# Kernel optimization log

Measured on AMD Instinct MI355X. Metric: run time of the kernel, lower is better.

The kernel has to match this reference:

```python
import jax, jax.numpy as jnp
import numpy as np

N_DRUG = 50000
N_PROT = 50000
N_EDGE = 800000
D_IN = 256
D_HID = 256
D_OUT = 128


def setup_inputs() -> dict:
    key = jax.random.key(0)
    ks = jax.random.split(key, 20)
    s_in = 1.0 / np.sqrt(D_IN)
    inp = {
        'x_drug': jax.random.normal(ks[0], (N_DRUG, D_IN), jnp.float32),
        'x_protein': jax.random.normal(ks[1], (N_PROT, D_IN), jnp.float32),
        'edge_dp': jnp.stack([
            jax.random.randint(ks[2], (N_EDGE,), 0, N_DRUG, jnp.int32),
            jax.random.randint(ks[3], (N_EDGE,), 0, N_PROT, jnp.int32)]),
        'edge_pd': jnp.stack([
            jax.random.randint(ks[4], (N_EDGE,), 0, N_PROT, jnp.int32),
            jax.random.randint(ks[5], (N_EDGE,), 0, N_DRUG, jnp.int32)]),
        'W1l_dp': jax.random.normal(ks[6], (D_IN, D_HID), jnp.float32) * s_in,
        'W1r_dp': jax.random.normal(ks[7], (D_IN, D_HID), jnp.float32) * s_in,
        'b1_dp': jnp.zeros((D_HID,), jnp.float32),
        'W1l_pd': jax.random.normal(ks[8], (D_IN, D_HID), jnp.float32) * s_in,
        'W1r_pd': jax.random.normal(ks[9], (D_IN, D_HID), jnp.float32) * s_in,
        'b1_pd': jnp.zeros((D_HID,), jnp.float32),
        'W2l_dp': jax.random.normal(ks[10], (D_HID, D_OUT), jnp.float32) / np.sqrt(D_HID),
        'W2r_dp': jax.random.normal(ks[11], (D_HID, D_OUT), jnp.float32) / np.sqrt(D_HID),
        'b2_dp': jnp.zeros((D_OUT,), jnp.float32),
        'W2l_pd': jax.random.normal(ks[12], (D_HID, D_OUT), jnp.float32) / np.sqrt(D_HID),
        'W2r_pd': jax.random.normal(ks[13], (D_HID, D_OUT), jnp.float32) / np.sqrt(D_HID),
        'b2_pd': jnp.zeros((D_OUT,), jnp.float32),
    }
    return inp


def _sage(x_src, x_dst, edge, Wl, Wr, b):
    """PyG SAGEConv (mean aggr): lin_l(mean_neighbors) + lin_r(x_dst) + bias."""
    src, dst = edge[0], edge[1]
    n_dst = x_dst.shape[0]
    msg = x_src[src]                                        # [E, d] gather
    s = jax.ops.segment_sum(msg, dst, num_segments=n_dst)   # [n_dst, d]
    cnt = jax.ops.segment_sum(jnp.ones((edge.shape[1],), x_src.dtype), dst,
                              num_segments=n_dst)
    mean = s / jnp.maximum(cnt, 1.0)[:, None]
    return mean @ Wl + x_dst @ Wr + b


def _l2norm(x, eps=1e-12):
    n = jnp.sqrt(jnp.sum(x * x, axis=-1, keepdims=True))
    return x / jnp.maximum(n, eps)


def reference(x_drug, x_protein, edge_dp, edge_pd,
              W1l_dp, W1r_dp, b1_dp, W1l_pd, W1r_pd, b1_pd,
              W2l_dp, W2r_dp, b2_dp, W2l_pd, W2r_pd, b2_pd):
    # Layer 1 (HeteroConv, aggr='sum'; each node type has one incoming edge type)
    h_prot = _sage(x_drug, x_protein, edge_dp, W1l_dp, W1r_dp, b1_dp)
    h_drug = _sage(x_protein, x_drug, edge_pd, W1l_pd, W1r_pd, b1_pd)
    h_prot = jax.nn.relu(h_prot)  # dropout is identity in eval mode
    h_drug = jax.nn.relu(h_drug)
    # Layer 2 (output layer) + L2 normalize
    z_prot = _sage(h_drug, h_prot, edge_dp, W2l_dp, W2r_dp, b2_dp)
    z_drug = _sage(h_prot, h_drug, edge_pd, W2l_pd, W2r_pd, b2_pd)
    return _l2norm(z_drug), _l2norm(z_prot)
```

## Files before the change

### kernel.cpp

```cpp
#include <hip/hip_runtime.h>

typedef unsigned short u16;
typedef unsigned int u32;
typedef __attribute__((ext_vector_type(8))) short short8;
typedef __attribute__((ext_vector_type(4))) float f32x4;

#define NDIM 256
#define KCAT 512
#define EB 8192
#define NBK_MAX 256

__device__ __forceinline__ float bf2f(u16 u) {
  union { u32 i; float f; } v; v.i = ((u32)u) << 16; return v.f;
}
__device__ __forceinline__ u16 f2bf(float f) {
  union { float f; u32 i; } v; v.f = f;
  u32 u = v.i;
  u32 r = (u + 0x7fffu + ((u >> 16) & 1u)) >> 16;
  return (u16)r;
}

__global__ void cvt_f32_bf16_2(const float* __restrict__ a, int n4a,
                               const float* __restrict__ b, int n4b,
                               u16* __restrict__ oa, u16* __restrict__ ob) {
  int i = blockIdx.x * blockDim.x + threadIdx.x;
  const float* in; u16* out; int j;
  if (i < n4a) { in = a; out = oa; j = i; }
  else { j = i - n4a; if (j >= n4b) return; in = b; out = ob; }
  const float4 v = reinterpret_cast<const float4*>(in)[j];
  u32 lo = (u32)f2bf(v.x) | ((u32)f2bf(v.y) << 16);
  u32 hi = (u32)f2bf(v.z) | ((u32)f2bf(v.w) << 16);
  reinterpret_cast<uint2*>(out)[j] = make_uint2(lo, hi);
}

__global__ void prep_wcat(const float* __restrict__ Wl0, const float* __restrict__ Wr0,
                          u16* __restrict__ WT0,
                          const float* __restrict__ Wl1, const float* __restrict__ Wr1,
                          u16* __restrict__ WT1) {
  int idx = blockIdx.x * blockDim.x + threadIdx.x;
  if (idx >= 256 * KCAT) return;
  const float* Wl = blockIdx.y ? Wl1 : Wl0;
  const float* Wr = blockIdx.y ? Wr1 : Wr0;
  u16* WT = blockIdx.y ? WT1 : WT0;
  int n = idx >> 9, k = idx & 511;
  float v = (k < 256) ? Wl[k * 256 + n] : Wr[(k - 256) * 256 + n];
  WT[idx] = f2bf(v);
}

__global__ void prep_wcat2(const float* __restrict__ Wl0, const float* __restrict__ Wr0,
                           u16* __restrict__ WT0,
                           const float* __restrict__ Wl1, const float* __restrict__ Wr1,
                           u16* __restrict__ WT1) {
  int idx = blockIdx.x * blockDim.x + threadIdx.x;
  if (idx >= 256 * 256) return;
  const float* Wl = blockIdx.y ? Wl1 : Wl0;
  const float* Wr = blockIdx.y ? Wr1 : Wr0;
  u16* WT = blockIdx.y ? WT1 : WT0;
  int n = idx >> 8, k = idx & 255;
  float v = (n < 128) ? Wl[k * 128 + n] : Wr[k * 128 + (n - 128)];
  WT[idx] = f2bf(v);
}

__global__ void prep_fbias(const float* __restrict__ bd, const float* __restrict__ bp,
                           float* __restrict__ fd, float* __restrict__ fp) {
  int n = threadIdx.x;
  fd[n] = (n < 128) ? 0.f : bd[n - 128];
  fp[n] = (n < 128) ? 0.f : bp[n - 128];
}

#define SCAN_CHUNK 2048

__global__ void scan_p1(const int* __restrict__ c0, int n0,
                        const int* __restrict__ c1, int n1,
                        int* __restrict__ bsums) {
  const int sel = blockIdx.y;
  const int* c = sel ? c1 : c0;
  const int n = sel ? n1 : n0;
  const int base = blockIdx.x * SCAN_CHUNK;
  const int tid = threadIdx.x, lane = tid & 63, w = tid >> 6;
  int s = 0;
  const int i0 = base + tid * 8;
#pragma unroll
  for (int j = 0; j < 8; ++j) {
    int i = i0 + j;
    s += (i < n) ? c[i] : 0;
  }
#pragma unroll
  for (int d = 1; d < 64; d <<= 1) s += __shfl_xor(s, d, 64);
  __shared__ int wsum[4];
  if (lane == 0) wsum[w] = s;
  __syncthreads();
  if (tid == 0) bsums[sel * 64 + blockIdx.x] = wsum[0] + wsum[1] + wsum[2] + wsum[3];
}

__global__ void scan_p2(int* __restrict__ bsums, int nb) {
  const int sel = blockIdx.x;
  const int lane = threadIdx.x;
  int v = (lane < nb) ? bsums[sel * 64 + lane] : 0;
#pragma unroll
  for (int d = 1; d < 64; d <<= 1) {
    int t = __shfl_up(v, d, 64);
    if (lane >= d) v += t;
  }
  int ex = __shfl_up(v, 1, 64);
  if (lane == 0) ex = 0;
  if (lane < nb) bsums[sel * 64 + lane] = ex;
}

__global__ void scan_p3(const int* __restrict__ c0, int n0, int* __restrict__ off0,
                        const int* __restrict__ c1, int n1, int* __restrict__ off1,
                        const int* __restrict__ bsums) {
  const int sel = blockIdx.y;
  const int* c = sel ? c1 : c0;
  int* off = sel ? off1 : off0;
  const int n = sel ? n1 : n0;
  const int base = blockIdx.x * SCAN_CHUNK;
  const int tid = threadIdx.x, lane = tid & 63, w = tid >> 6;
  int v[8];
  int s = 0;
  const int i0 = base + tid * 8;
#pragma unroll
  for (int j = 0; j < 8; ++j) {
    int i = i0 + j;
    v[j] = (i < n) ? c[i] : 0;
    s += v[j];
  }
  int inc = s;
#pragma unroll
  for (int d = 1; d < 64; d <<= 1) {
    int t = __shfl_up(inc, d, 64);
    if (lane >= d) inc += t;
  }
  __shared__ int wsum[4];
  if (lane == 63) wsum[w] = inc;
  __syncthreads();
  int wbase = 0;
  for (int q = 0; q < w; ++q) wbase += wsum[q];
  int run = (inc - s) + wbase + bsums[sel * 64 + blockIdx.x];
#pragma unroll
  for (int j = 0; j < 8; ++j) {
    int i = i0 + j;
    run += v[j];
    if (i < n) off[i + 1] = run;
  }
  if (blockIdx.x == 0 && tid == 0) off[0] = 0;
}

__global__ void hist_pass(const int* __restrict__ d0, const int* __restrict__ d1, int E,
                          int nblk, int nbuckets, int* __restrict__ h0, int* __restrict__ h1) {
  const int sel = blockIdx.y;
  const int* dst = sel ? d1 : d0;
  int* hist = sel ? h1 : h0;
  const int blk = blockIdx.x;
  __shared__ int h[NBK_MAX];
  for (int b = threadIdx.x; b < nbuckets; b += 256) h[b] = 0;
  __syncthreads();
  const int e0 = blk * EB;
  const int e1 = (e0 + EB < E) ? (e0 + EB) : E;
  for (int i = e0 + threadIdx.x; i < e1; i += 256) atomicAdd(&h[dst[i] >> 8], 1);
  __syncthreads();
  for (int b = threadIdx.x; b < nbuckets; b += 256) hist[b * nblk + blk] = h[b];
}

__global__ void part_pass(const int* __restrict__ s0, const int* __restrict__ d0, u32* __restrict__ t0,
                          const int* __restrict__ s1, const int* __restrict__ d1, u32* __restrict__ t1,
                          const int* __restrict__ ho0, const int* __restrict__ ho1,
                          int E, int nblk, int nbuckets) {
  const int sel = blockIdx.y;
  const int* src = sel ? s1 : s0;
  const int* dst = sel ? d1 : d0;
  const int* hoff = sel ? ho1 : ho0;
  u32* tmp = sel ? t1 : t0;
  const int blk = blockIdx.x;
  __shared__ int cur[NBK_MAX];
  for (int b = threadIdx.x; b < nbuckets; b += 256) cur[b] = hoff[b * nblk + blk];
  __syncthreads();
  const int e0 = blk * EB;
  const int e1 = (e0 + EB < E) ? (e0 + EB) : E;
  for (int i = e0 + threadIdx.x; i < e1; i += 256) {
    const int d = dst[i];
    const int p = atomicAdd(&cur[d >> 8], 1);
    tmp[p] = ((u32)(d & 255) << 16) | (u32)src[i];
  }
}

__global__ void bucket_fill(const u32* __restrict__ t0, const int* __restrict__ ho0,
                            int n0, int* __restrict__ off0, int* __restrict__ l0,
                            const u32* __restrict__ t1, const int* __restrict__ ho1,
                            int n1, int* __restrict__ off1, int* __restrict__ l1,
                            int E, int nblk, int nbuckets) {
  const int sel = blockIdx.y;
  const u32* tmp = sel ? t1 : t0;
  const int* hoff = sel ? ho1 : ho0;
  const int n = sel ? n1 : n0;
  int* off = sel ? off1 : off0;
  int* lst = sel ? l1 : l0;
  const int b = blockIdx.x;
  const int node0 = b << 8;
  if (node0 >= n) return;
  const int nodes = (n - node0 < 256) ? (n - node0) : 256;
  const int base = hoff[b * nblk];
  const int bend = hoff[(b + 1) * nblk];
  const int t = threadIdx.x, lane = t & 63, w = t >> 6;
  __shared__ int cnt[256];
  __shared__ int wsum[4];
  cnt[t] = 0;
  __syncthreads();
  for (int i = base + t; i < bend; i += 256) atomicAdd(&cnt[tmp[i] >> 16], 1);
  __syncthreads();
  const int v = cnt[t];
  int inc = v;
#pragma unroll
  for (int d = 1; d < 64; d <<= 1) {
    int x = __shfl_up(inc, d, 64);
    if (lane >= d) inc += x;
  }
  if (lane == 63) wsum[w] = inc;
  __syncthreads();
  int wb = 0;
  for (int q = 0; q < w; ++q) wb += wsum[q];
  const int excl = base + (inc - v) + wb;
  __syncthreads();
  cnt[t] = excl;
  if (t < nodes) off[node0 + t] = excl;
  if (node0 + nodes == n && t == 0) off[n] = E;
  __syncthreads();
  for (int i = base + t; i < bend; i += 256) {
    const u32 pk = tmp[i];
    const int p = atomicAdd(&cnt[pk >> 16], 1);
    lst[p] = (int)(pk & 0xffffu);
  }
}

__global__ void seg_mean(const u16* __restrict__ f0, const int* __restrict__ o0,
                         const int* __restrict__ l0, u16* __restrict__ out0, int n0,
                         const u16* __restrict__ f1, const int* __restrict__ o1,
                         const int* __restrict__ l1, u16* __restrict__ out1, int n1) {
  const int sel = blockIdx.y;
  const u16* feat = sel ? f1 : f0;
  const int* off = sel ? o1 : o0;
  const int* lst = sel ? l1 : l0;
  u16* out = sel ? out1 : out0;
  const int ndst = sel ? n1 : n0;
  const int wid = threadIdx.x >> 6, lane = threadIdx.x & 63;
  const int node = blockIdx.x * 4 + wid;
  if (node >= ndst) return;
  const int s = off[node], e = off[node + 1];
  const int half = lane >> 5, hl = lane & 31;
  float a[8];
#pragma unroll
  for (int j = 0; j < 8; ++j) a[j] = 0.f;
  int i = s;
  for (; i + 8 <= e; i += 8) {
    const int q0 = lst[i + half], q1 = lst[i + 2 + half];
    const int q2 = lst[i + 4 + half], q3 = lst[i + 6 + half];
    const uint4 v0 = *reinterpret_cast<const uint4*>(feat + (size_t)q0 * NDIM + hl * 8);
    const uint4 v1 = *reinterpret_cast<const uint4*>(feat + (size_t)q1 * NDIM + hl * 8);
    const uint4 v2 = *reinterpret_cast<const uint4*>(feat + (size_t)q2 * NDIM + hl * 8);
    const uint4 v3 = *reinterpret_cast<const uint4*>(feat + (size_t)q3 * NDIM + hl * 8);
    const u32 w0[4] = {v0.x, v0.y, v0.z, v0.w};
    const u32 w1[4] = {v1.x, v1.y, v1.z, v1.w};
    const u32 w2[4] = {v2.x, v2.y, v2.z, v2.w};
    const u32 w3[4] = {v3.x, v3.y, v3.z, v3.w};
#pragma unroll
    for (int q = 0; q < 4; ++q) {
      a[2 * q] += bf2f((u16)(w0[q] & 0xffffu)) + bf2f((u16)(w1[q] & 0xffffu)) +
                  bf2f((u16)(w2[q] & 0xffffu)) + bf2f((u16)(w3[q] & 0xffffu));
      a[2 * q + 1] += bf2f((u16)(w0[q] >> 16)) + bf2f((u16)(w1[q] >> 16)) +
                      bf2f((u16)(w2[q] >> 16)) + bf2f((u16)(w3[q] >> 16));
    }
  }
  for (; i < e; i += 2) {
    if (i + half < e) {
      const int q = lst[i + half];
      const uint4 v = *reinterpret_cast<const uint4*>(feat + (size_t)q * NDIM + hl * 8);
      const u32 w[4] = {v.x, v.y, v.z, v.w};
#pragma unroll
      for (int t = 0; t < 4; ++t) {
        a[2 * t] += bf2f((u16)(w[t] & 0xffffu));
        a[2 * t + 1] += bf2f((u16)(w[t] >> 16));
      }
    }
  }
#pragma unroll
  for (int j = 0; j < 8; ++j) a[j] += __shfl_xor(a[j], 32, 64);
  if (half == 0) {
    const float inv = (e > s) ? 1.f / (float)(e - s) : 0.f;
    uint4 o;
    o.x = (u32)f2bf(a[0] * inv) | ((u32)f2bf(a[1] * inv) << 16);
    o.y = (u32)f2bf(a[2] * inv) | ((u32)f2bf(a[3] * inv) << 16);
    o.z = (u32)f2bf(a[4] * inv) | ((u32)f2bf(a[5] * inv) << 16);
    o.w = (u32)f2bf(a[6] * inv) | ((u32)f2bf(a[7] * inv) << 16);
    *reinterpret_cast<uint4*>(out + (size_t)node * NDIM + hl * 8) = o;
  }
}

__global__ void seg_out(const u16* __restrict__ ym0, const u16* __restrict__ ys0,
                        const int* __restrict__ o0, const int* __restrict__ l0,
                        float* __restrict__ z0, int n0,
                        const u16* __restrict__ ym1, const u16* __restrict__ ys1,
                        const int* __restrict__ o1, const int* __restrict__ l1,
                        float* __restrict__ z1, int n1) {
  const int sel = blockIdx.y;
  const u16* ymsg = sel ? ym1 : ym0;
  const u16* yself = sel ? ys1 : ys0;
  const int* off = sel ? o1 : o0;
  const int* lst = sel ? l1 : l0;
  float* zout = sel ? z1 : z0;
  const int ndst = sel ? n1 : n0;
  const int wid = threadIdx.x >> 6, lane = threadIdx.x & 63;
  const int node = blockIdx.x * 4 + wid;
  if (node >= ndst) return;
  const int s = off[node], e = off[node + 1];
  const int q = lane >> 4, ql = lane & 15;
  float a[8];
#pragma unroll
  for (int j = 0; j < 8; ++j) a[j] = 0.f;
  int i = s;
  for (; i + 8 <= e; i += 8) {
    const int r0 = lst[i + q], r1 = lst[i + 4 + q];
    const uint4 v0 = *reinterpret_cast<const uint4*>(ymsg + (size_t)r0 * 128 + ql * 8);
    const uint4 v1 = *reinterpret_cast<const uint4*>(ymsg + (size_t)r1 * 128 + ql * 8);
    const u32 w0[4] = {v0.x, v0.y, v0.z, v0.w};
    const u32 w1[4] = {v1.x, v1.y, v1.z, v1.w};
#pragma unroll
    for (int c = 0; c < 4; ++c) {
      a[2 * c] += bf2f((u16)(w0[c] & 0xffffu)) + bf2f((u16)(w1[c] & 0xffffu));
      a[2 * c + 1] += bf2f((u16)(w0[c] >> 16)) + bf2f((u16)(w1[c] >> 16));
    }
  }
  for (; i + 4 <= e; i += 4) {
    const int r = lst[i + q];
    const uint4 v = *reinterpret_cast<const uint4*>(ymsg + (size_t)r * 128 + ql * 8);
    const u32 w[4] = {v.x, v.y, v.z, v.w};
#pragma unroll
    for (int c = 0; c < 4; ++c) {
      a[2 * c] += bf2f((u16)(w[c] & 0xffffu));
      a[2 * c + 1] += bf2f((u16)(w[c] >> 16));
    }
  }
  if (i + q < e) {
    const int r = lst[i + q];
    const uint4 v = *reinterpret_cast<const uint4*>(ymsg + (size_t)r * 128 + ql * 8);
    const u32 w[4] = {v.x, v.y, v.z, v.w};
#pragma unroll
    for (int c = 0; c < 4; ++c) {
      a[2 * c] += bf2f((u16)(w[c] & 0xffffu));
      a[2 * c + 1] += bf2f((u16)(w[c] >> 16));
    }
  }
#pragma unroll
  for (int j = 0; j < 8; ++j) {
    a[j] += __shfl_xor(a[j], 16, 64);
    a[j] += __shfl_xor(a[j], 32, 64);
  }
  const float inv = (e > s) ? 1.f / (float)(e - s) : 0.f;
  const uint4 r = *reinterpret_cast<const uint4*>(yself + (size_t)node * 128 + ql * 8);
  const u32 rw[4] = {r.x, r.y, r.z, r.w};
  float z[8];
  float ss = 0.f;
#pragma unroll
  for (int c = 0; c < 4; ++c) {
    z[2 * c] = a[2 * c] * inv + bf2f((u16)(rw[c] & 0xffffu));
    z[2 * c + 1] = a[2 * c + 1] * inv + bf2f((u16)(rw[c] >> 16));
    ss += z[2 * c] * z[2 * c] + z[2 * c + 1] * z[2 * c + 1];
  }
#pragma unroll
  for (int d = 1; d < 16; d <<= 1) ss += __shfl_xor(ss, d, 64);
  const float sc = 1.f / fmaxf(sqrtf(ss), 1e-12f);
  if (q == 0) {
    float4 o0v, o1v;
    o0v.x = z[0] * sc; o0v.y = z[1] * sc; o0v.z = z[2] * sc; o0v.w = z[3] * sc;
    o1v.x = z[4] * sc; o1v.y = z[5] * sc; o1v.z = z[6] * sc; o1v.w = z[7] * sc;
    float* zp = zout + (size_t)node * 128 + ql * 8;
    *reinterpret_cast<float4*>(zp) = o0v;
    *reinterpret_cast<float4*>(zp + 4) = o1v;
  }
}

template <bool RELU, bool CAT, int KT, bool SPLIT>
__global__ __launch_bounds__(256) void gemm2(
    const u16* __restrict__ Am0, const u16* __restrict__ Ax0,
    const u16* __restrict__ WT0, const float* __restrict__ bias0,
    u16* __restrict__ out0, u16* __restrict__ outs0, int M0,
    const u16* __restrict__ Am1, const u16* __restrict__ Ax1,
    const u16* __restrict__ WT1, const float* __restrict__ bias1,
    u16* __restrict__ out1, u16* __restrict__ outs1, int M1,
    int gx, int ldb, int ldo) {
  const int raw = blockIdx.x;
  const int xcd = raw & 7, seq = raw >> 3;
  const int ny = seq & 1;
  const int mt = (seq >> 1) * 8 + xcd;
  if (mt >= gx) return;
  const int sel = blockIdx.z;
  const u16* Am = sel ? Am1 : Am0;
  const u16* Ax = sel ? Ax1 : Ax0;
  const u16* WT = sel ? WT1 : WT0;
  const float* bias = sel ? bias1 : bias0;
  u16* out = sel ? out1 : out0;
  u16* outs = sel ? outs1 : outs0;
  const int M = sel ? M1 : M0;
  const int gm0 = mt * 128;
  if (gm0 >= M) return;
  const int n0 = ny * 128;

  __shared__ u16 As[8192];
  __shared__ u16 Bs[8192];
  const int tid = threadIdx.x;
  const int wid = tid >> 6, lane = tid & 63;
  const int wr = wid >> 1, wc = wid & 1;

  f32x4 acc[4][4];
  const f32x4 zz = {0.f, 0.f, 0.f, 0.f};
#pragma unroll
  for (int i = 0; i < 4; ++i)
#pragma unroll
    for (int j = 0; j < 4; ++j) acc[i][j] = zz;

  for (int kt = 0; kt < KT; ++kt) {
    const u16* Asrc = CAT ? ((kt < KT / 2) ? Am : Ax) : Am;
    const int koff = CAT ? ((kt & (KT / 2 - 1)) * 64) : kt * 64;
#pragma unroll
    for (int t = 0; t < 4; ++t) {
      const int f = wid * 256 + t * 64 + lane;
      const int row = f >> 3;
      const int ch = (f & 7) ^ (row & 7);
      int grow = gm0 + row; grow = (grow < M) ? grow : (M - 1);
      const u16* g = Asrc + (size_t)grow * NDIM + koff + ch * 8;
      u16* l = &As[(size_t)f * 8];
      __builtin_amdgcn_global_load_lds((const __attribute__((address_space(1))) void*)g,
                                       (__attribute__((address_space(3))) void*)l, 16, 0, 0);
    }
#pragma unroll
    for (int t = 0; t < 4; ++t) {
      const int f = wid * 256 + t * 64 + lane;
      const int n = f >> 3;
      const int ch = (f & 7) ^ (n & 7);
      const u16* g = WT + (size_t)(n0 + n) * ldb + kt * 64 + ch * 8;
      u16* l = &Bs[(size_t)f * 8];
      __builtin_amdgcn_global_load_lds((const __attribute__((address_space(1))) void*)g,
                                       (__attribute__((address_space(3))) void*)l, 16, 0, 0);
    }
    __syncthreads();
#pragma unroll
    for (int ks = 0; ks < 2; ++ks) {
      const int kc = ks * 4 + (lane >> 4);
      short8 a[4], b[4];
#pragma unroll
      for (int mtt = 0; mtt < 4; ++mtt) {
        const int R = wr * 64 + mtt * 16 + (lane & 15);
        a[mtt] = *reinterpret_cast<const short8*>(&As[(size_t)R * 64 + (kc ^ (R & 7)) * 8]);
      }
#pragma unroll
      for (int nt = 0; nt < 4; ++nt) {
        const int N = wc * 64 + nt * 16 + (lane & 15);
        b[nt] = *reinterpret_cast<const short8*>(&Bs[(size_t)N * 64 + (kc ^ (N & 7)) * 8]);
      }
#pragma unroll
      for (int mtt = 0; mtt < 4; ++mtt)
#pragma unroll
        for (int nt = 0; nt < 4; ++nt)
          acc[mtt][nt] = __builtin_amdgcn_mfma_f32_16x16x32_bf16(a[mtt], b[nt], acc[mtt][nt], 0, 0, 0);
    }
    __syncthreads();
  }

  const int rw = gm0 + wr * 64;
#pragma unroll
  for (int mtt = 0; mtt < 4; ++mtt) {
#pragma unroll
    for (int j = 0; j < 4; ++j) {
      int row = rw + mtt * 16 + ((lane >> 4) << 2) + j;
      if (row >= M) continue;
#pragma unroll
      for (int nt = 0; nt < 4; ++nt) {
        int col = n0 + wc * 64 + nt * 16 + (lane & 15);
        float v = acc[mtt][nt][j] + bias[col];
        if (RELU) v = fmaxf(v, 0.f);
        if constexpr (SPLIT) {
          if (col < 128) out[(size_t)row * 128 + col] = f2bf(v);
          else outs[(size_t)row * 128 + col - 128] = f2bf(v);
        } else {
          out[(size_t)row * ldo + col] = f2bf(v);
        }
      }
    }
  }
}

extern "C" void kernel_launch(void* const* d_in, const int* in_sizes, int n_in,
                              void* d_out, int out_size, void* d_ws, size_t ws_size,
                              hipStream_t stream) {
  const float* x_drug = (const float*)d_in[0];
  const float* x_prot = (const float*)d_in[1];
  const int* e_dp = (const int*)d_in[2];
  const int* e_pd = (const int*)d_in[3];
  const float* W1l_dp = (const float*)d_in[4];
  const float* W1r_dp = (const float*)d_in[5];
  const float* b1_dp = (const float*)d_in[6];
  const float* W1l_pd = (const float*)d_in[7];
  const float* W1r_pd = (const float*)d_in[8];
  const float* b1_pd = (const float*)d_in[9];
  const float* W2l_dp = (const float*)d_in[10];
  const float* W2r_dp = (const float*)d_in[11];
  const float* b2_dp = (const float*)d_in[12];
  const float* W2l_pd = (const float*)d_in[13];
  const float* W2r_pd = (const float*)d_in[14];
  const float* b2_pd = (const float*)d_in[15];

  const int E = in_sizes[2] / 2;
  const int ND = in_sizes[0] / NDIM;
  const int NP = in_sizes[1] / NDIM;

  const int* dp_src = e_dp;
  const int* dp_dst = e_dp + E;
  const int* pd_src = e_pd;
  const int* pd_dst = e_pd + E;

  char* ws = (char*)d_ws;
  size_t o = 0;
  auto alloc = [&](size_t bytes) -> void* {
    void* p = ws + o;
    o = (o + bytes + 255) & ~(size_t)255;
    return p;
  };
  u16* xd16 = (u16*)alloc((size_t)ND * NDIM * 2);
  u16* xp16 = (u16*)alloc((size_t)NP * NDIM * 2);
  u16* mp16 = (u16*)alloc((size_t)NP * NDIM * 2);
  u16* md16 = (u16*)alloc((size_t)ND * NDIM * 2);
  u16* hp16 = (u16*)alloc((size_t)NP * NDIM * 2);
  u16* hd16 = (u16*)alloc((size_t)ND * NDIM * 2);
  u16* wt1dp = (u16*)alloc((size_t)256 * KCAT * 2);
  u16* wt1pd = (u16*)alloc((size_t)256 * KCAT * 2);
  u16* wt2d = (u16*)alloc((size_t)256 * 256 * 2);
  u16* wt2p = (u16*)alloc((size_t)256 * 256 * 2);
  float* fbias_d = (float*)alloc(256 * 4);
  float* fbias_p = (float*)alloc(256 * 4);
  int* off_dp = (int*)alloc((size_t)(NP + 1) * 4);
  int* off_pd = (int*)alloc((size_t)(ND + 1) * 4);
  int* bsums2 = (int*)alloc((size_t)2 * 64 * 4);
  int* lst_dp = (int*)alloc((size_t)E * 4);
  int* lst_pd = (int*)alloc((size_t)E * 4);
  u32* tmp_dp = (u32*)alloc((size_t)E * 4);
  u32* tmp_pd = (u32*)alloc((size_t)E * 4);

  const int nmax = (NP > ND) ? NP : ND;
  const int nbuckets = (nmax + 255) >> 8;
  const int nblk = (E + EB - 1) / EB;
  const int nh = nbuckets * nblk;
  int* hist0 = (int*)alloc((size_t)nh * 4);
  int* hist1 = (int*)alloc((size_t)nh * 4);
  int* hoff0 = (int*)alloc((size_t)(nh + 1) * 4);
  int* hoff1 = (int*)alloc((size_t)(nh + 1) * 4);

  dim3 blk(256);

  const int n4d = ND * NDIM / 4, n4p = NP * NDIM / 4;
  cvt_f32_bf16_2<<<(n4d + n4p + 255) / 256, blk, 0, stream>>>(x_drug, n4d, x_prot, n4p, xd16, xp16);

  prep_wcat<<<dim3((256 * KCAT + 255) / 256, 2), blk, 0, stream>>>(
      W1l_dp, W1r_dp, wt1dp, W1l_pd, W1r_pd, wt1pd);
  prep_wcat2<<<dim3((256 * 256 + 255) / 256, 2), blk, 0, stream>>>(
      W2l_dp, W2r_pd, wt2d, W2l_pd, W2r_dp, wt2p);
  prep_fbias<<<1, 256, 0, stream>>>(b2_pd, b2_dp, fbias_d, fbias_p);

  hist_pass<<<dim3(nblk, 2), blk, 0, stream>>>(dp_dst, pd_dst, E, nblk, nbuckets, hist0, hist1);
  const int nb2 = (nh + SCAN_CHUNK - 1) / SCAN_CHUNK;
  dim3 sg2(nb2, 2);
  scan_p1<<<sg2, blk, 0, stream>>>(hist0, nh, hist1, nh, bsums2);
  scan_p2<<<2, 64, 0, stream>>>(bsums2, nb2);
  scan_p3<<<sg2, blk, 0, stream>>>(hist0, nh, hoff0, hist1, nh, hoff1, bsums2);
  part_pass<<<dim3(nblk, 2), blk, 0, stream>>>(
      dp_src, dp_dst, tmp_dp, pd_src, pd_dst, tmp_pd, hoff0, hoff1, E, nblk, nbuckets);
  bucket_fill<<<dim3(nbuckets, 2), blk, 0, stream>>>(
      tmp_dp, hoff0, NP, off_dp, lst_dp, tmp_pd, hoff1, ND, off_pd, lst_pd, E, nblk, nbuckets);

  seg_mean<<<dim3((nmax + 3) / 4, 2), blk, 0, stream>>>(
      xd16, off_dp, lst_dp, mp16, NP, xp16, off_pd, lst_pd, md16, ND);

  const int gx = (nmax + 127) / 128;
  const int gridx = ((gx + 7) / 8) * 16;

  gemm2<true, true, 8, false><<<dim3(gridx, 1, 2), blk, 0, stream>>>(
      mp16, xp16, wt1dp, b1_dp, hp16, (u16*)nullptr, NP,
      md16, xd16, wt1pd, b1_pd, hd16, (u16*)nullptr, ND, gx, KCAT, 256);

  u16* ymsg_d = md16;
  u16* yself_d = md16 + (size_t)ND * 128;
  u16* ymsg_p = mp16;
  u16* yself_p = mp16 + (size_t)NP * 128;
  gemm2<false, false, 4, true><<<dim3(gridx, 1, 2), blk, 0, stream>>>(
      hd16, hd16, wt2d, fbias_d, ymsg_d, yself_d, ND,
      hp16, hp16, wt2p, fbias_p, ymsg_p, yself_p, NP, gx, 256, 256);

  float* zd = (float*)d_out;
  float* zp = zd + (size_t)ND * 128;
  seg_out<<<dim3((nmax + 3) / 4, 2), blk, 0, stream>>>(
      ymsg_p, yself_d, off_pd, lst_pd, zd, ND, ymsg_d, yself_p, off_dp, lst_dp, zp, NP);
}
```

Before: 380.2 us.

## Merge setup kernels, use a single-block scan, and double-buffer GEMM LDS

Folds the bf16 conversion, the weight packing, the bias prep and the destination histogram into one launch, with block ranges selecting the role. The three-kernel histogram scan becomes one 1024-thread block per edge type. The GEMM now stages the next K tile into a second LDS buffer while the MFMAs run on the current one. This removes several kernel launches and the serialization between them, and hides global-to-LDS load latency. In exchange the GEMM uses twice the LDS per block, which may lower occupancy, and the single-block scan does serial work.

```diff
diff --git a/kernel.cpp b/kernel.cpp
--- a/kernel.cpp
+++ b/kernel.cpp
@@ -20,146 +20,102 @@
   return (u16)r;
 }
 
-__global__ void cvt_f32_bf16_2(const float* __restrict__ a, int n4a,
-                               const float* __restrict__ b, int n4b,
-                               u16* __restrict__ oa, u16* __restrict__ ob) {
-  int i = blockIdx.x * blockDim.x + threadIdx.x;
-  const float* in; u16* out; int j;
-  if (i < n4a) { in = a; out = oa; j = i; }
-  else { j = i - n4a; if (j >= n4b) return; in = b; out = ob; }
-  const float4 v = reinterpret_cast<const float4*>(in)[j];
-  u32 lo = (u32)f2bf(v.x) | ((u32)f2bf(v.y) << 16);
-  u32 hi = (u32)f2bf(v.z) | ((u32)f2bf(v.w) << 16);
-  reinterpret_cast<uint2*>(out)[j] = make_uint2(lo, hi);
-}
-
-__global__ void prep_wcat(const float* __restrict__ Wl0, const float* __restrict__ Wr0,
-                          u16* __restrict__ WT0,
-                          const float* __restrict__ Wl1, const float* __restrict__ Wr1,
-                          u16* __restrict__ WT1) {
-  int idx = blockIdx.x * blockDim.x + threadIdx.x;
-  if (idx >= 256 * KCAT) return;
-  const float* Wl = blockIdx.y ? Wl1 : Wl0;
-  const float* Wr = blockIdx.y ? Wr1 : Wr0;
-  u16* WT = blockIdx.y ? WT1 : WT0;
-  int n = idx >> 9, k = idx & 511;
-  float v = (k < 256) ? Wl[k * 256 + n] : Wr[(k - 256) * 256 + n];
-  WT[idx] = f2bf(v);
-}
-
-__global__ void prep_wcat2(const float* __restrict__ Wl0, const float* __restrict__ Wr0,
-                           u16* __restrict__ WT0,
-                           const float* __restrict__ Wl1, const float* __restrict__ Wr1,
-                           u16* __restrict__ WT1) {
-  int idx = blockIdx.x * blockDim.x + threadIdx.x;
-  if (idx >= 256 * 256) return;
-  const float* Wl = blockIdx.y ? Wl1 : Wl0;
-  const float* Wr = blockIdx.y ? Wr1 : Wr0;
-  u16* WT = blockIdx.y ? WT1 : WT0;
-  int n = idx >> 8, k = idx & 255;
-  float v = (n < 128) ? Wl[k * 128 + n] : Wr[k * 128 + (n - 128)];
-  WT[idx] = f2bf(v);
-}
-
-__global__ void prep_fbias(const float* __restrict__ bd, const float* __restrict__ bp,
-                           float* __restrict__ fd, float* __restrict__ fp) {
-  int n = threadIdx.x;
-  fd[n] = (n < 128) ? 0.f : bd[n - 128];
-  fp[n] = (n < 128) ? 0.f : bp[n - 128];
-}
-
-#define SCAN_CHUNK 2048
-
-__global__ void scan_p1(const int* __restrict__ c0, int n0,
-                        const int* __restrict__ c1, int n1,
-                        int* __restrict__ bsums) {
-  const int sel = blockIdx.y;
-  const int* c = sel ? c1 : c0;
-  const int n = sel ? n1 : n0;
-  const int base = blockIdx.x * SCAN_CHUNK;
-  const int tid = threadIdx.x, lane = tid & 63, w = tid >> 6;
+__global__ void setup_all(
+    const float* __restrict__ xd, int n4d, const float* __restrict__ xp, int n4p,
+    u16* __restrict__ xd16, u16* __restrict__ xp16,
+    const float* __restrict__ W1l0, const float* __restrict__ W1r0, u16* __restrict__ WT10,
+    const float* __restrict__ W1l1, const float* __restrict__ W1r1, u16* __restrict__ WT11,
+    const float* __restrict__ W2l0, const float* __restrict__ W2r0, u16* __restrict__ WT20,
+    const float* __restrict__ W2l1, const float* __restrict__ W2r1, u16* __restrict__ WT21,
+    const float* __restrict__ b2d, const float* __restrict__ b2p,
+    float* __restrict__ fd, float* __restrict__ fp,
+    const int* __restrict__ dpd, const int* __restrict__ pdd, int E,
+    int nblk, int nbuckets, int* __restrict__ h0, int* __restrict__ h1,
+    int tA, int tB, int tC, int tD) {
+  __shared__ int h[NBK_MAX];
+  const int b = blockIdx.x;
+  const int tid = threadIdx.x;
+  if (b < tA) {
+    int i = b * 256 + tid;
+    const float* in; u16* out; int j;
+    if (i < n4d) { in = xd; out = xd16; j = i; }
+    else { j = i - n4d; if (j >= n4p) return; in = xp; out = xp16; }
+    const float4 v = reinterpret_cast<const float4*>(in)[j];
+    u32 lo = (u32)f2bf(v.x) | ((u32)f2bf(v.y) << 16);
+    u32 hi = (u32)f2bf(v.z) | ((u32)f2bf(v.w) << 16);
+    reinterpret_cast<uint2*>(out)[j] = make_uint2(lo, hi);
+  } else if (b < tB) {
+    int gidx = (b - tA) * 256 + tid;
+    const int sel = gidx >> 17;
+    const int idx = gidx & 131071;
+    const float* Wl = sel ? W1l1 : W1l0;
+    const float* Wr = sel ? W1r1 : W1r0;
+    u16* WT = sel ? WT11 : WT10;
+    int n = idx >> 9, k = idx & 511;
+    float v = (k < 256) ? Wl[k * 256 + n] : Wr[(k - 256) * 256 + n];
+    WT[idx] = f2bf(v);
+  } else if (b < tC) {
+    int gidx = (b - tB) * 256 + tid;
+    const int sel = gidx >> 16;
+    const int idx = gidx & 65535;
+    const float* Wl = sel ? W2l1 : W2l0;
+    const float* Wr = sel ? W2r1 : W2r0;
+    u16* WT = sel ? WT21 : WT20;
+    int n = idx >> 8, k = idx & 255;
+    float v = (n < 128) ? Wl[k * 128 + n] : Wr[k * 128 + (n - 128)];
+    WT[idx] = f2bf(v);
+  } else if (b < tD) {
+    fd[tid] = (tid < 128) ? 0.f : b2d[tid - 128];
+    fp[tid] = (tid < 128) ? 0.f : b2p[tid - 128];
+  } else {
+    const int hb = b - tD;
+    const int sel = (hb >= nblk);
+    const int blk = sel ? hb - nblk : hb;
+    const int* dst = sel ? pdd : dpd;
+    int* hist = sel ? h1 : h0;
+    for (int x = tid; x < nbuckets; x += 256) h[x] = 0;
+    __syncthreads();
+    const int e0 = blk * EB;
+    const int e1 = (e0 + EB < E) ? (e0 + EB) : E;
+    for (int i = e0 + tid; i < e1; i += 256) atomicAdd(&h[dst[i] >> 8], 1);
+    __syncthreads();
+    for (int x = tid; x < nbuckets; x += 256) hist[x * nblk + blk] = h[x];
+  }
+}
+
+#define SCAN_PER 20
+__global__ void scan_one(const int* __restrict__ h0, int* __restrict__ o0,
+                         const int* __restrict__ h1, int* __restrict__ o1, int nh) {
+  const int sel = blockIdx.x;
+  const int* h = sel ? h1 : h0;
+  int* off = sel ? o1 : o0;
+  const int tid = threadIdx.x;
+  int v[SCAN_PER];
   int s = 0;
-  const int i0 = base + tid * 8;
-#pragma unroll
-  for (int j = 0; j < 8; ++j) {
+  const int i0 = tid * SCAN_PER;
+#pragma unroll
+  for (int j = 0; j < SCAN_PER; ++j) {
     int i = i0 + j;
-    s += (i < n) ? c[i] : 0;
-  }
-#pragma unroll
-  for (int d = 1; d < 64; d <<= 1) s += __shfl_xor(s, d, 64);
-  __shared__ int wsum[4];
-  if (lane == 0) wsum[w] = s;
-  __syncthreads();
-  if (tid == 0) bsums[sel * 64 + blockIdx.x] = wsum[0] + wsum[1] + wsum[2] + wsum[3];
-}
-
-__global__ void scan_p2(int* __restrict__ bsums, int nb) {
-  const int sel = blockIdx.x;
-  const int lane = threadIdx.x;
-  int v = (lane < nb) ? bsums[sel * 64 + lane] : 0;
-#pragma unroll
-  for (int d = 1; d < 64; d <<= 1) {
-    int t = __shfl_up(v, d, 64);
-    if (lane >= d) v += t;
-  }
-  int ex = __shfl_up(v, 1, 64);
-  if (lane == 0) ex = 0;
-  if (lane < nb) bsums[sel * 64 + lane] = ex;
-}
-
-__global__ void scan_p3(const int* __restrict__ c0, int n0, int* __restrict__ off0,
-                        const int* __restrict__ c1, int n1, int* __restrict__ off1,
-                        const int* __restrict__ bsums) {
-  const int sel = blockIdx.y;
-  const int* c = sel ? c1 : c0;
-  int* off = sel ? off1 : off0;
-  const int n = sel ? n1 : n0;
-  const int base = blockIdx.x * SCAN_CHUNK;
-  const int tid = threadIdx.x, lane = tid & 63, w = tid >> 6;
-  int v[8];
-  int s = 0;
-  const int i0 = base + tid * 8;
-#pragma unroll
-  for (int j = 0; j < 8; ++j) {
-    int i = i0 + j;
-    v[j] = (i < n) ? c[i] : 0;
+    v[j] = (i < nh) ? h[i] : 0;
     s += v[j];
   }
-  int inc = s;
-#pragma unroll
-  for (int d = 1; d < 64; d <<= 1) {
-    int t = __shfl_up(inc, d, 64);
-    if (lane >= d) inc += t;
-  }
-  __shared__ int wsum[4];
-  if (lane == 63) wsum[w] = inc;
-  __syncthreads();
-  int wbase = 0;
-  for (int q = 0; q < w; ++q) wbase += wsum[q];
-  int run = (inc - s) + wbase + bsums[sel * 64 + blockIdx.x];
-#pragma unroll
-  for (int j = 0; j < 8; ++j) {
+  __shared__ int tile[1024];
+  tile[tid] = s;
+  __syncthreads();
+  for (int d = 1; d < 1024; d <<= 1) {
+    int t = (tid >= d) ? tile[tid - d] : 0;
+    __syncthreads();
+    tile[tid] += t;
+    __syncthreads();
+  }
+  int run = tile[tid] - s;
+#pragma unroll
+  for (int j = 0; j < SCAN_PER; ++j) {
     int i = i0 + j;
     run += v[j];
-    if (i < n) off[i + 1] = run;
-  }
-  if (blockIdx.x == 0 && tid == 0) off[0] = 0;
-}
-
-__global__ void hist_pass(const int* __restrict__ d0, const int* __restrict__ d1, int E,
-                          int nblk, int nbuckets, int* __restrict__ h0, int* __restrict__ h1) {
-  const int sel = blockIdx.y;
-  const int* dst = sel ? d1 : d0;
-  int* hist = sel ? h1 : h0;
-  const int blk = blockIdx.x;
-  __shared__ int h[NBK_MAX];
-  for (int b = threadIdx.x; b < nbuckets; b += 256) h[b] = 0;
-  __syncthreads();
-  const int e0 = blk * EB;
-  const int e1 = (e0 + EB < E) ? (e0 + EB) : E;
-  for (int i = e0 + threadIdx.x; i < e1; i += 256) atomicAdd(&h[dst[i] >> 8], 1);
-  __syncthreads();
-  for (int b = threadIdx.x; b < nbuckets; b += 256) hist[b * nblk + blk] = h[b];
+    if (i < nh) off[i + 1] = run;
+  }
+  if (tid == 0) off[0] = 0;
 }
 
 __global__ void part_pass(const int* __restrict__ s0, const int* __restrict__ d0, u32* __restrict__ t0,
@@ -404,8 +360,8 @@
   if (gm0 >= M) return;
   const int n0 = ny * 128;
 
-  __shared__ u16 As[8192];
-  __shared__ u16 Bs[8192];
+  __shared__ u16 As[2][8192];
+  __shared__ u16 Bs[2][8192];
   const int tid = threadIdx.x;
   const int wid = tid >> 6, lane = tid & 63;
   const int wr = wid >> 1, wc = wid & 1;
@@ -417,7 +373,7 @@
 #pragma unroll
     for (int j = 0; j < 4; ++j) acc[i][j] = zz;
 
-  for (int kt = 0; kt < KT; ++kt) {
+  auto stage = [&](int kt, int buf) {
     const u16* Asrc = CAT ? ((kt < KT / 2) ? Am : Ax) : Am;
     const int koff = CAT ? ((kt & (KT / 2 - 1)) * 64) : kt * 64;
 #pragma unroll
@@ -427,7 +383,7 @@
       const int ch = (f & 7) ^ (row & 7);
       int grow = gm0 + row; grow = (grow < M) ? grow : (M - 1);
       const u16* g = Asrc + (size_t)grow * NDIM + koff + ch * 8;
-      u16* l = &As[(size_t)f * 8];
+      u16* l = &As[buf][(size_t)f * 8];
       __builtin_amdgcn_global_load_lds((const __attribute__((address_space(1))) void*)g,
                                        (__attribute__((address_space(3))) void*)l, 16, 0, 0);
     }
@@ -437,11 +393,18 @@
       const int n = f >> 3;
       const int ch = (f & 7) ^ (n & 7);
       const u16* g = WT + (size_t)(n0 + n) * ldb + kt * 64 + ch * 8;
-      u16* l = &Bs[(size_t)f * 8];
+      u16* l = &Bs[buf][(size_t)f * 8];
       __builtin_amdgcn_global_load_lds((const __attribute__((address_space(1))) void*)g,
                                        (__attribute__((address_space(3))) void*)l, 16, 0, 0);
     }
-    __syncthreads();
+  };
+
+  stage(0, 0);
+  __syncthreads();
+
+  for (int kt = 0; kt < KT; ++kt) {
+    const int cur = kt & 1;
+    if (kt + 1 < KT) stage(kt + 1, cur ^ 1);
 #pragma unroll
     for (int ks = 0; ks < 2; ++ks) {
       const int kc = ks * 4 + (lane >> 4);
@@ -449,12 +412,12 @@
 #pragma unroll
       for (int mtt = 0; mtt < 4; ++mtt) {
         const int R = wr * 64 + mtt * 16 + (lane & 15);
-        a[mtt] = *reinterpret_cast<const short8*>(&As[(size_t)R * 64 + (kc ^ (R & 7)) * 8]);
+        a[mtt] = *reinterpret_cast<const short8*>(&As[cur][(size_t)R * 64 + (kc ^ (R & 7)) * 8]);
       }
 #pragma unroll
       for (int nt = 0; nt < 4; ++nt) {
         const int N = wc * 64 + nt * 16 + (lane & 15);
-        b[nt] = *reinterpret_cast<const short8*>(&Bs[(size_t)N * 64 + (kc ^ (N & 7)) * 8]);
+        b[nt] = *reinterpret_cast<const short8*>(&Bs[cur][(size_t)N * 64 + (kc ^ (N & 7)) * 8]);
       }
 #pragma unroll
       for (int mtt = 0; mtt < 4; ++mtt)
@@ -538,7 +501,6 @@
   float* fbias_p = (float*)alloc(256 * 4);
   int* off_dp = (int*)alloc((size_t)(NP + 1) * 4);
   int* off_pd = (int*)alloc((size_t)(ND + 1) * 4);
-  int* bsums2 = (int*)alloc((size_t)2 * 64 * 4);
   int* lst_dp = (int*)alloc((size_t)E * 4);
   int* lst_pd = (int*)alloc((size_t)E * 4);
   u32* tmp_dp = (u32*)alloc((size_t)E * 4);
@@ -556,20 +518,21 @@
   dim3 blk(256);
 
   const int n4d = ND * NDIM / 4, n4p = NP * NDIM / 4;
-  cvt_f32_bf16_2<<<(n4d + n4p + 255) / 256, blk, 0, stream>>>(x_drug, n4d, x_prot, n4p, xd16, xp16);
-
-  prep_wcat<<<dim3((256 * KCAT + 255) / 256, 2), blk, 0, stream>>>(
-      W1l_dp, W1r_dp, wt1dp, W1l_pd, W1r_pd, wt1pd);
-  prep_wcat2<<<dim3((256 * 256 + 255) / 256, 2), blk, 0, stream>>>(
-      W2l_dp, W2r_pd, wt2d, W2l_pd, W2r_dp, wt2p);
-  prep_fbias<<<1, 256, 0, stream>>>(b2_pd, b2_dp, fbias_d, fbias_p);
-
-  hist_pass<<<dim3(nblk, 2), blk, 0, stream>>>(dp_dst, pd_dst, E, nblk, nbuckets, hist0, hist1);
-  const int nb2 = (nh + SCAN_CHUNK - 1) / SCAN_CHUNK;
-  dim3 sg2(nb2, 2);
-  scan_p1<<<sg2, blk, 0, stream>>>(hist0, nh, hist1, nh, bsums2);
-  scan_p2<<<2, 64, 0, stream>>>(bsums2, nb2);
-  scan_p3<<<sg2, blk, 0, stream>>>(hist0, nh, hoff0, hist1, nh, hoff1, bsums2);
+  const int tA = (n4d + n4p + 255) / 256;
+  const int tB = tA + (2 * 256 * KCAT + 255) / 256;
+  const int tC = tB + (2 * 256 * 256 + 255) / 256;
+  const int tD = tC + 1;
+  const int tTotal = tD + 2 * nblk;
+  setup_all<<<tTotal, blk, 0, stream>>>(
+      x_drug, n4d, x_prot, n4p, xd16, xp16,
+      W1l_dp, W1r_dp, wt1dp, W1l_pd, W1r_pd, wt1pd,
+      W2l_dp, W2r_pd, wt2d, W2l_pd, W2r_dp, wt2p,
+      b2_pd, b2_dp, fbias_d, fbias_p,
+      dp_dst, pd_dst, E, nblk, nbuckets, hist0, hist1,
+      tA, tB, tC, tD);
+
+  scan_one<<<2, 1024, 0, stream>>>(hist0, hoff0, hist1, hoff1, nh);
+
   part_pass<<<dim3(nblk, 2), blk, 0, stream>>>(
       dp_src, dp_dst, tmp_dp, pd_src, pd_dst, tmp_pd, hoff0, hoff1, E, nblk, nbuckets);
   bucket_fill<<<dim3(nbuckets, 2), blk, 0, stream>>>(
```

Measured after the change: 388.9 us. 1.02x slower.
